# Kernel tuning notes

Measured on AMD Instinct MI355X. Metric: run time of the kernel, lower is better.

Reference implementation:

```python
import jax, jax.numpy as jnp
import numpy as np

B, S, D, H = 2, 4096, 512, 4
HD = D // H          # head_dim = key_size = value_size = 128
BLK = 512            # mask_block_size (tri-block-diagonal mask)


def setup_inputs() -> dict:
    key = jax.random.key(0)
    ks = jax.random.split(key, 7)
    # tri-block-diagonal boolean mask: query block attends to itself and adjacent blocks
    blk = np.arange(S) // BLK
    mask = np.abs(blk[:, None] - blk[None, :]) <= 1
    w_scale = 1.0 / np.sqrt(D)  # ~ variance_scaling fan_in init magnitude
    return {
        "q_input": jax.random.normal(ks[0], (B, S, D), jnp.float32),
        "kv_input": jax.random.normal(ks[1], (B, S, D), jnp.float32),
        "Wq": jax.random.normal(ks[2], (D, H * HD), jnp.float32) * w_scale,
        "Wk": jax.random.normal(ks[3], (D, H * HD), jnp.float32) * w_scale,
        "Wv": jax.random.normal(ks[4], (D, H * HD), jnp.float32) * w_scale,
        "Wo": jax.random.normal(ks[5], (H * HD, D), jnp.float32) * w_scale,
        "bo": jnp.zeros((D,), jnp.float32),
        "mask": jnp.asarray(mask),
    }


def reference(q_input, kv_input, Wq, Wk, Wv, Wo, bo, mask):
    b, s, _ = q_input.shape
    # multihead projections -> [b, s, H, HD]
    q = (q_input @ Wq).reshape(b, s, H, HD)
    k = (kv_input @ Wk).reshape(b, s, H, HD)
    v = (kv_input @ Wv).reshape(b, s, H, HD)
    # normalize_q=True: scale by key_size**-0.5 (no tanh soft cap)
    q = q * (HD ** -0.5)
    # masked attention (splash attention math): [b, H, sq, sk]
    scores = jnp.einsum("bqhd,bkhd->bhqk", q, k)
    neg = jnp.finfo(scores.dtype).min
    scores = jnp.where(mask[None, None], scores, neg)
    p = jax.nn.softmax(scores, axis=-1)
    out = jnp.einsum("bhqk,bkhd->bqhd", p, v)
    out = out.reshape(b, s, H * HD)
    return out @ Wo + bo
```

## Files before the change

kernel.cpp:

```cpp
#include <hip/hip_runtime.h>
#include <hip/hip_bf16.h>

#define S_LEN 4096
#define D_MODEL 512
#define NHEADS 4
#define HEAD_DIM 128
#define BATCH 2
#define M_ROWS 8192

typedef unsigned short u16;
typedef __attribute__((ext_vector_type(8))) short bf16x8;
typedef __attribute__((ext_vector_type(4))) short bf16x4;
typedef __attribute__((ext_vector_type(4))) float f32x4;

__device__ __forceinline__ float bf2f(u16 u) {
    return __uint_as_float(((unsigned)u) << 16);
}
__device__ __forceinline__ short f2b(float f) {
    unsigned x = __float_as_uint(f);
    unsigned r = (x + 0x7fffu + ((x >> 16) & 1u)) >> 16;
    return (short)r;
}

__device__ __forceinline__ int detect_f32(const u16* u, int nelem, int tid, int* s_cnt) {
    if (tid == 0) *s_cnt = 0;
    __syncthreads();
    int samp = nelem < 4096 ? nelem : 4096;
    int c = 0;
    for (int i = tid; i < samp; i += 256) {
        float af = fabsf(bf2f(u[i]));
        if (af != 0.0f && (!(af <= 1e12f) || af < 1e-12f)) c++;
    }
    atomicAdd(s_cnt, c);
    __syncthreads();
    return *s_cnt > 16;
}

__global__ __launch_bounds__(256) void prep_w(const void* w0, const void* w1,
                                              const void* w2, const void* w3, u16* wt) {
    __shared__ int s_cnt;
    __shared__ float tile[32][33];
    const int tid = threadIdx.x;
    const int wi = blockIdx.x >> 8, t = blockIdx.x & 255;
    const void* W = (wi == 0) ? w0 : (wi == 1) ? w1 : (wi == 2) ? w2 : w3;
    const int f32 = detect_f32((const u16*)W, 262144, tid, &s_cnt);
    const float scale = (wi == 0) ? 0.0883883476483184f : 1.0f;
    u16* Wt = wt + (size_t)wi * D_MODEL * D_MODEL;
    const int k0 = (t >> 4) * 32, n0 = (t & 15) * 32;
    const int tx = tid & 31, ty = tid >> 5;
#pragma unroll
    for (int i = 0; i < 4; i++) {
        int r = ty + 8 * i;
        long long off = (long long)(k0 + r) * D_MODEL + n0 + tx;
        float v = f32 ? ((const float*)W)[off] : bf2f(((const u16*)W)[off]);
        tile[r][tx] = v * scale;
    }
    __syncthreads();
#pragma unroll
    for (int i = 0; i < 4; i++) {
        int r = ty + 8 * i;
        Wt[(size_t)(n0 + r) * D_MODEL + k0 + tx] = (u16)f2b(tile[tx][r]);
    }
}

__global__ __launch_bounds__(256) void proj_mfma(const void* qin, const void* kvin,
                                                 const u16* wt, u16* qb, u16* kb,
                                                 u16* vbT) {
    __shared__ int s_cnt;
    __shared__ short As[128][72];
    __shared__ short Ws[128][72];
    const int z = blockIdx.z;
    const void* A = (z == 0) ? qin : kvin;
    const u16* Wt = wt + (size_t)z * 262144;
    const int tid = threadIdx.x;
    const int f32a = detect_f32((const u16*)A, 4194304, tid, &s_cnt);
    const int row0 = blockIdx.x * 128, col0 = blockIdx.y * 128;
    const int srow = tid >> 1, sk0 = (tid & 1) * 32;
    const int lane = tid & 63, wid = tid >> 6;
    const int wm = wid >> 1, wn = wid & 1;
    const int l16 = lane & 15, quad = lane >> 4;

    f32x4 acc[4][4];
#pragma unroll
    for (int i = 0; i < 4; i++)
#pragma unroll
        for (int j = 0; j < 4; j++) acc[i][j] = (f32x4){0.f, 0.f, 0.f, 0.f};

    for (int k0 = 0; k0 < D_MODEL; k0 += 64) {
        if (f32a) {
            const float* ap = (const float*)A + (size_t)(row0 + srow) * D_MODEL + k0 + sk0;
            short s[32];
#pragma unroll
            for (int i = 0; i < 8; i++) {
                f32x4 t = *(const f32x4*)(ap + 4 * i);
                s[4 * i] = f2b(t.x); s[4 * i + 1] = f2b(t.y);
                s[4 * i + 2] = f2b(t.z); s[4 * i + 3] = f2b(t.w);
            }
#pragma unroll
            for (int i = 0; i < 4; i++)
                *(bf16x8*)&As[srow][sk0 + 8 * i] = *(bf16x8*)(s + 8 * i);
        } else {
            const u16* ap = (const u16*)A + (size_t)(row0 + srow) * D_MODEL + k0 + sk0;
#pragma unroll
            for (int i = 0; i < 4; i++)
                *(bf16x8*)&As[srow][sk0 + 8 * i] = *(const bf16x8*)(ap + 8 * i);
        }
        {
            const u16* wp = Wt + (size_t)(col0 + srow) * D_MODEL + k0 + sk0;
#pragma unroll
            for (int i = 0; i < 4; i++)
                *(bf16x8*)&Ws[srow][sk0 + 8 * i] = *(const bf16x8*)(wp + 8 * i);
        }
        __syncthreads();
#pragma unroll
        for (int kc = 0; kc < 2; kc++) {
            bf16x8 af[4], bfr[4];
#pragma unroll
            for (int i = 0; i < 4; i++)
                af[i] = *(const bf16x8*)&As[wm * 64 + i * 16 + l16][kc * 32 + quad * 8];
#pragma unroll
            for (int j = 0; j < 4; j++)
                bfr[j] = *(const bf16x8*)&Ws[wn * 64 + j * 16 + l16][kc * 32 + quad * 8];
#pragma unroll
            for (int i = 0; i < 4; i++)
#pragma unroll
                for (int j = 0; j < 4; j++)
                    acc[i][j] = __builtin_amdgcn_mfma_f32_16x16x32_bf16(af[i], bfr[j],
                                                                       acc[i][j], 0, 0, 0);
        }
        __syncthreads();
    }
    if (z == 2) {
#pragma unroll
        for (int i = 0; i < 4; i++) {
            int grow = row0 + wm * 64 + i * 16 + quad * 4;
            int b = grow >> 12, s = grow & (S_LEN - 1);
#pragma unroll
            for (int j = 0; j < 4; j++) {
                int gcol = col0 + wn * 64 + j * 16 + l16;
                int h = gcol >> 7, d = gcol & 127;
                short v[4];
#pragma unroll
                for (int r = 0; r < 4; r++) v[r] = f2b(acc[i][j][r]);
                *(bf16x4*)&vbT[((size_t)(b * NHEADS + h) * HEAD_DIM + d) * S_LEN + s] =
                    *(bf16x4*)v;
            }
        }
    } else {
        u16* out = (z == 0) ? qb : kb;
#pragma unroll
        for (int i = 0; i < 4; i++) {
            int grow = row0 + wm * 64 + i * 16 + quad * 4;
#pragma unroll
            for (int j = 0; j < 4; j++) {
                int gcol = col0 + wn * 64 + j * 16 + l16;
                int h = gcol >> 7, d = gcol & 127;
#pragma unroll
                for (int r = 0; r < 4; r++) {
                    int row = grow + r;
                    int b = row >> 12, s = row & (S_LEN - 1);
                    out[((size_t)(b * NHEADS + h) * S_LEN + s) * HEAD_DIM + d] =
                        (u16)f2b(acc[i][j][r]);
                }
            }
        }
    }
}

__global__ __launch_bounds__(256, 3) void attn_mfma(const u16* qb, const u16* kb,
                                                    const u16* vbT, u16* op0, u16* op1,
                                                    u16* op2, float* lp) {
    __shared__ short Ks[32][136];
    __shared__ short Vs[128][40];
    const int bid = blockIdx.x;
    const int bh = bid & 7;
    const int rest = bid >> 3;
    const int qt = rest / 3;
    const int p3 = rest - qt * 3;
    const int q0 = qt << 7;
    const int qblk = q0 >> 9;
    const int kstart0 = (qblk == 0) ? 0 : ((qblk - 1) << 9);
    const int kend0 = (qblk == 7) ? S_LEN : ((qblk + 2) << 9);
    const int kcount = kend0 - kstart0;
    const int third = (kcount / 3) & ~31;
    const int rem32 = (kcount - 3 * third) >> 5;
    const int kstart = kstart0 + p3 * third + (p3 < rem32 ? p3 : rem32) * 32;
    const int klen = third + (p3 < rem32 ? 32 : 0);
    const int tid = threadIdx.x;
    const int lane = tid & 63, wid = tid >> 6;
    const int l16 = lane & 15, quad = lane >> 4;
    const u16* qp = qb + (size_t)bh * S_LEN * HEAD_DIM;
    const u16* kp = kb + (size_t)bh * S_LEN * HEAD_DIM;
    const u16* vp = vbT + (size_t)bh * HEAD_DIM * S_LEN;

    bf16x8 qf[2][4];
    {
        const int r = tid >> 3, c0 = (tid & 7) * 16;
        for (int c = 0; c < 4; c++) {
            const u16* src = qp + (size_t)(q0 + c * 32 + r) * HEAD_DIM + c0;
            *(bf16x8*)&Ks[r][c0] = *(const bf16x8*)src;
            *(bf16x8*)&Ks[r][c0 + 8] = *(const bf16x8*)(src + 8);
            __syncthreads();
            if (wid == c) {
#pragma unroll
                for (int i = 0; i < 2; i++)
#pragma unroll
                    for (int kc = 0; kc < 4; kc++)
                        qf[i][kc] = *(const bf16x8*)&Ks[i * 16 + l16][kc * 32 + quad * 8];
            }
            __syncthreads();
        }
    }

    f32x4 o[2][8], lacc[2];
#pragma unroll
    for (int i = 0; i < 2; i++) {
        lacc[i] = (f32x4){0.f, 0.f, 0.f, 0.f};
#pragma unroll
        for (int n = 0; n < 8; n++) o[i][n] = (f32x4){0.f, 0.f, 0.f, 0.f};
    }
    bf16x8 ones;
#pragma unroll
    for (int t = 0; t < 8; t++) ones[t] = (short)0x3F80;

    const int krow = tid >> 3, kc0 = (tid & 7) * 16;
    const int kperm = ((krow >> 2) & 1) * 16 + (krow >> 3) * 4 + (krow & 3);
    const int vd = tid >> 1, vc0 = (tid & 1) * 16;

    for (int kk = 0; kk < klen; kk += 32) {
        const int kt = kstart + kk;
        __syncthreads();
        {
            const u16* src = kp + (size_t)(kt + krow) * HEAD_DIM + kc0;
            *(bf16x8*)&Ks[kperm][kc0] = *(const bf16x8*)src;
            *(bf16x8*)&Ks[kperm][kc0 + 8] = *(const bf16x8*)(src + 8);
        }
        {
            const u16* src = vp + (size_t)vd * S_LEN + kt + vc0;
            *(bf16x8*)&Vs[vd][vc0] = *(const bf16x8*)src;
            *(bf16x8*)&Vs[vd][vc0 + 8] = *(const bf16x8*)(src + 8);
        }
        __syncthreads();
        f32x4 sa[2][2];
#pragma unroll
        for (int ki = 0; ki < 2; ki++)
#pragma unroll
            for (int qi = 0; qi < 2; qi++) sa[ki][qi] = (f32x4){0.f, 0.f, 0.f, 0.f};
#pragma unroll
        for (int kc = 0; kc < 4; kc++) {
            bf16x8 kf0 = *(const bf16x8*)&Ks[l16][kc * 32 + quad * 8];
            bf16x8 kf1 = *(const bf16x8*)&Ks[16 + l16][kc * 32 + quad * 8];
#pragma unroll
            for (int qi = 0; qi < 2; qi++) {
                sa[0][qi] = __builtin_amdgcn_mfma_f32_16x16x32_bf16(kf0, qf[qi][kc], sa[0][qi], 0, 0, 0);
                sa[1][qi] = __builtin_amdgcn_mfma_f32_16x16x32_bf16(kf1, qf[qi][kc], sa[1][qi], 0, 0, 0);
            }
        }
        bf16x8 pfrag[2];
#pragma unroll
        for (int qi = 0; qi < 2; qi++) {
            short pv[8];
#pragma unroll
            for (int ki = 0; ki < 2; ki++)
#pragma unroll
                for (int r = 0; r < 4; r++)
                    pv[ki * 4 + r] = f2b(__expf(sa[ki][qi][r] - 8.0f));
            pfrag[qi] = *(bf16x8*)pv;
            lacc[qi] = __builtin_amdgcn_mfma_f32_16x16x32_bf16(ones, pfrag[qi], lacc[qi], 0, 0, 0);
        }
#pragma unroll
        for (int n = 0; n < 8; n++) {
            bf16x8 vf = *(const bf16x8*)&Vs[n * 16 + l16][quad * 8];
#pragma unroll
            for (int qi = 0; qi < 2; qi++)
                o[qi][n] = __builtin_amdgcn_mfma_f32_16x16x32_bf16(vf, pfrag[qi], o[qi][n], 0, 0, 0);
        }
    }
    u16* op = (p3 == 0) ? op0 : (p3 == 1 ? op1 : op2);
#pragma unroll
    for (int qi = 0; qi < 2; qi++) {
        size_t gq = (size_t)bh * S_LEN + q0 + wid * 32 + qi * 16 + l16;
#pragma unroll
        for (int n = 0; n < 8; n++) {
            short v[4];
#pragma unroll
            for (int r = 0; r < 4; r++) v[r] = f2b(o[qi][n][r]);
            *(bf16x4*)&op[gq * HEAD_DIM + n * 16 + quad * 4] = *(bf16x4*)v;
        }
        if (quad == 0) lp[(size_t)p3 * 8 * S_LEN + gq] = lacc[qi][0];
    }
}

__global__ __launch_bounds__(256) void outproj_mfma(const u16* op0, const u16* op1,
                                                    const u16* op2, const float* lp,
                                                    const u16* Wt, const void* bias,
                                                    float* out) {
    __shared__ int s_cnt;
    __shared__ short As[64][72];
    __shared__ short Ws[128][72];
    const int tid = threadIdx.x;
    const int f32b = detect_f32((const u16*)bias, 512, tid, &s_cnt);
    const int row0 = blockIdx.x * 64, col0 = blockIdx.y * 128;
    const int lane = tid & 63, wid = tid >> 6;
    const int wm = wid >> 1, wn = wid & 1;
    const int l16 = lane & 15, quad = lane >> 4;
    const int sr = tid >> 2, sk = (tid & 3) * 16;
    const int wr = tid >> 1, wk = (tid & 1) * 32;
    const size_t N = (size_t)8 * S_LEN;
    const int arow = row0 + sr;
    const int ab = arow >> 12, as = arow & (S_LEN - 1);
    f32x4 acc[2][4];
#pragma unroll
    for (int i = 0; i < 2; i++)
#pragma unroll
        for (int j = 0; j < 4; j++) acc[i][j] = (f32x4){0.f, 0.f, 0.f, 0.f};

    for (int k0 = 0; k0 < D_MODEL; k0 += 64) {
        {
            const int h = (k0 + sk) >> 7, d = (k0 + sk) & 127;
            const size_t gq = (size_t)(ab * NHEADS + h) * S_LEN + as;
            float inv = 1.0f / (lp[gq] + lp[N + gq] + lp[2 * N + gq]);
            const size_t base = gq * HEAD_DIM + d;
            bf16x8 a0 = *(const bf16x8*)&op0[base];
            bf16x8 a1 = *(const bf16x8*)&op1[base];
            bf16x8 a2 = *(const bf16x8*)&op2[base];
            bf16x8 b0 = *(const bf16x8*)&op0[base + 8];
            bf16x8 b1 = *(const bf16x8*)&op1[base + 8];
            bf16x8 b2 = *(const bf16x8*)&op2[base + 8];
            short v[16];
#pragma unroll
            for (int i = 0; i < 8; i++) {
                v[i] = f2b((bf2f((u16)a0[i]) + bf2f((u16)a1[i]) + bf2f((u16)a2[i])) * inv);
                v[8 + i] = f2b((bf2f((u16)b0[i]) + bf2f((u16)b1[i]) + bf2f((u16)b2[i])) * inv);
            }
            *(bf16x8*)&As[sr][sk] = *(bf16x8*)v;
            *(bf16x8*)&As[sr][sk + 8] = *(bf16x8*)(v + 8);
        }
        {
            const u16* wp = Wt + (size_t)(col0 + wr) * D_MODEL + k0 + wk;
#pragma unroll
            for (int i = 0; i < 4; i++)
                *(bf16x8*)&Ws[wr][wk + 8 * i] = *(const bf16x8*)(wp + 8 * i);
        }
        __syncthreads();
#pragma unroll
        for (int kc = 0; kc < 2; kc++) {
            bf16x8 af[2], bfr[4];
#pragma unroll
            for (int i = 0; i < 2; i++)
                af[i] = *(const bf16x8*)&As[wm * 32 + i * 16 + l16][kc * 32 + quad * 8];
#pragma unroll
            for (int j = 0; j < 4; j++)
                bfr[j] = *(const bf16x8*)&Ws[wn * 64 + j * 16 + l16][kc * 32 + quad * 8];
#pragma unroll
            for (int i = 0; i < 2; i++)
#pragma unroll
                for (int j = 0; j < 4; j++)
                    acc[i][j] = __builtin_amdgcn_mfma_f32_16x16x32_bf16(af[i], bfr[j],
                                                                       acc[i][j], 0, 0, 0);
        }
        __syncthreads();
    }
#pragma unroll
    for (int i = 0; i < 2; i++) {
        int grow = row0 + wm * 32 + i * 16 + quad * 4;
#pragma unroll
        for (int j = 0; j < 4; j++) {
            int gcol = col0 + wn * 64 + j * 16 + l16;
            float bval = f32b ? ((const float*)bias)[gcol] : bf2f(((const u16*)bias)[gcol]);
#pragma unroll
            for (int r = 0; r < 4; r++)
                out[(size_t)(grow + r) * D_MODEL + gcol] = acc[i][j][r] + bval;
        }
    }
}

extern "C" void kernel_launch(void* const* d_in, const int* in_sizes, int n_in,
                              void* d_out, int out_size, void* d_ws, size_t ws_size,
                              hipStream_t stream) {
    (void)in_sizes; (void)out_size; (void)ws_size; (void)n_in;
    const void* q_input = d_in[0];
    const void* kv_input = d_in[1];
    const void* Wq = d_in[2];
    const void* Wk = d_in[3];
    const void* Wv = d_in[4];
    const void* Wo = d_in[5];
    const void* bo = d_in[6];

    const size_t NELEM = (size_t)M_ROWS * D_MODEL;
    u16* wt = (u16*)d_ws;
    u16* qb = wt + 4 * 262144;
    u16* kb = qb + NELEM;
    u16* vbT = kb + NELEM;
    u16* op0 = vbT + NELEM;
    u16* op1 = op0 + NELEM;
    u16* op2 = op1 + NELEM;
    float* lp = (float*)(op2 + NELEM);

    prep_w<<<1024, 256, 0, stream>>>(Wq, Wk, Wv, Wo, wt);
    proj_mfma<<<dim3(64, 4, 3), 256, 0, stream>>>(q_input, kv_input, wt, qb, kb, vbT);
    attn_mfma<<<8 * 32 * 3, 256, 0, stream>>>(qb, kb, vbT, op0, op1, op2, lp);
    outproj_mfma<<<dim3(128, 4), 256, 0, stream>>>(op0, op1, op2, lp, wt + 3 * 262144,
                                                   bo, (float*)d_out);
}
```

Measured before the change: 246.8 us.

## Halve projection row tile and double attention key tile to 64

The projection GEMM now uses 64-row tiles instead of 128, doubling the grid to 1536 blocks so more CUs are occupied. The attention kernel processes 64 keys per iteration instead of 32, using larger K/V shared tiles and two score groups per step. This halves the number of barriers and tile loads in the attention loop. In exchange it raises LDS and register use, which could reduce occupancy under launch_bounds(256,3), and the smaller projection tile reuses each weight tile across fewer rows.

New measurement: 229.8 us. 1.07x faster.

```diff
diff --git a/kernel.cpp b/kernel.cpp
--- a/kernel.cpp
+++ b/kernel.cpp
@@ -67,62 +67,61 @@
                                                  const u16* wt, u16* qb, u16* kb,
                                                  u16* vbT) {
     __shared__ int s_cnt;
-    __shared__ short As[128][72];
+    __shared__ short As[64][72];
     __shared__ short Ws[128][72];
     const int z = blockIdx.z;
     const void* A = (z == 0) ? qin : kvin;
     const u16* Wt = wt + (size_t)z * 262144;
     const int tid = threadIdx.x;
     const int f32a = detect_f32((const u16*)A, 4194304, tid, &s_cnt);
-    const int row0 = blockIdx.x * 128, col0 = blockIdx.y * 128;
-    const int srow = tid >> 1, sk0 = (tid & 1) * 32;
+    const int row0 = blockIdx.x * 64, col0 = blockIdx.y * 128;
     const int lane = tid & 63, wid = tid >> 6;
     const int wm = wid >> 1, wn = wid & 1;
     const int l16 = lane & 15, quad = lane >> 4;
-
-    f32x4 acc[4][4];
-#pragma unroll
-    for (int i = 0; i < 4; i++)
+    const int ar = tid >> 2, ak = (tid & 3) * 16;
+    const int wr = tid >> 1, wk = (tid & 1) * 32;
+
+    f32x4 acc[2][4];
+#pragma unroll
+    for (int i = 0; i < 2; i++)
 #pragma unroll
         for (int j = 0; j < 4; j++) acc[i][j] = (f32x4){0.f, 0.f, 0.f, 0.f};
 
     for (int k0 = 0; k0 < D_MODEL; k0 += 64) {
         if (f32a) {
-            const float* ap = (const float*)A + (size_t)(row0 + srow) * D_MODEL + k0 + sk0;
-            short s[32];
-#pragma unroll
-            for (int i = 0; i < 8; i++) {
+            const float* ap = (const float*)A + (size_t)(row0 + ar) * D_MODEL + k0 + ak;
+            short s[16];
+#pragma unroll
+            for (int i = 0; i < 4; i++) {
                 f32x4 t = *(const f32x4*)(ap + 4 * i);
                 s[4 * i] = f2b(t.x); s[4 * i + 1] = f2b(t.y);
                 s[4 * i + 2] = f2b(t.z); s[4 * i + 3] = f2b(t.w);
             }
+            *(bf16x8*)&As[ar][ak] = *(bf16x8*)s;
+            *(bf16x8*)&As[ar][ak + 8] = *(bf16x8*)(s + 8);
+        } else {
+            const u16* ap = (const u16*)A + (size_t)(row0 + ar) * D_MODEL + k0 + ak;
+            *(bf16x8*)&As[ar][ak] = *(const bf16x8*)ap;
+            *(bf16x8*)&As[ar][ak + 8] = *(const bf16x8*)(ap + 8);
+        }
+        {
+            const u16* wp = Wt + (size_t)(col0 + wr) * D_MODEL + k0 + wk;
 #pragma unroll
             for (int i = 0; i < 4; i++)
-                *(bf16x8*)&As[srow][sk0 + 8 * i] = *(bf16x8*)(s + 8 * i);
-        } else {
-            const u16* ap = (const u16*)A + (size_t)(row0 + srow) * D_MODEL + k0 + sk0;
-#pragma unroll
-            for (int i = 0; i < 4; i++)
-                *(bf16x8*)&As[srow][sk0 + 8 * i] = *(const bf16x8*)(ap + 8 * i);
-        }
-        {
-            const u16* wp = Wt + (size_t)(col0 + srow) * D_MODEL + k0 + sk0;
-#pragma unroll
-            for (int i = 0; i < 4; i++)
-                *(bf16x8*)&Ws[srow][sk0 + 8 * i] = *(const bf16x8*)(wp + 8 * i);
+                *(bf16x8*)&Ws[wr][wk + 8 * i] = *(const bf16x8*)(wp + 8 * i);
         }
         __syncthreads();
 #pragma unroll
         for (int kc = 0; kc < 2; kc++) {
-            bf16x8 af[4], bfr[4];
-#pragma unroll
-            for (int i = 0; i < 4; i++)
-                af[i] = *(const bf16x8*)&As[wm * 64 + i * 16 + l16][kc * 32 + quad * 8];
+            bf16x8 af[2], bfr[4];
+#pragma unroll
+            for (int i = 0; i < 2; i++)
+                af[i] = *(const bf16x8*)&As[wm * 32 + i * 16 + l16][kc * 32 + quad * 8];
 #pragma unroll
             for (int j = 0; j < 4; j++)
                 bfr[j] = *(const bf16x8*)&Ws[wn * 64 + j * 16 + l16][kc * 32 + quad * 8];
 #pragma unroll
-            for (int i = 0; i < 4; i++)
+            for (int i = 0; i < 2; i++)
 #pragma unroll
                 for (int j = 0; j < 4; j++)
                     acc[i][j] = __builtin_amdgcn_mfma_f32_16x16x32_bf16(af[i], bfr[j],
@@ -132,8 +131,8 @@
     }
     if (z == 2) {
 #pragma unroll
-        for (int i = 0; i < 4; i++) {
-            int grow = row0 + wm * 64 + i * 16 + quad * 4;
+        for (int i = 0; i < 2; i++) {
+            int grow = row0 + wm * 32 + i * 16 + quad * 4;
             int b = grow >> 12, s = grow & (S_LEN - 1);
 #pragma unroll
             for (int j = 0; j < 4; j++) {
@@ -149,8 +148,8 @@
     } else {
         u16* out = (z == 0) ? qb : kb;
 #pragma unroll
-        for (int i = 0; i < 4; i++) {
-            int grow = row0 + wm * 64 + i * 16 + quad * 4;
+        for (int i = 0; i < 2; i++) {
+            int grow = row0 + wm * 32 + i * 16 + quad * 4;
 #pragma unroll
             for (int j = 0; j < 4; j++) {
                 int gcol = col0 + wn * 64 + j * 16 + l16;
@@ -170,8 +169,8 @@
 __global__ __launch_bounds__(256, 3) void attn_mfma(const u16* qb, const u16* kb,
                                                     const u16* vbT, u16* op0, u16* op1,
                                                     u16* op2, float* lp) {
-    __shared__ short Ks[32][136];
-    __shared__ short Vs[128][40];
+    __shared__ short Ks[64][136];
+    __shared__ short Vs[128][72];
     const int bid = blockIdx.x;
     const int bh = bid & 7;
     const int rest = bid >> 3;
@@ -182,10 +181,10 @@
     const int kstart0 = (qblk == 0) ? 0 : ((qblk - 1) << 9);
     const int kend0 = (qblk == 7) ? S_LEN : ((qblk + 2) << 9);
     const int kcount = kend0 - kstart0;
-    const int third = (kcount / 3) & ~31;
-    const int rem32 = (kcount - 3 * third) >> 5;
-    const int kstart = kstart0 + p3 * third + (p3 < rem32 ? p3 : rem32) * 32;
-    const int klen = third + (p3 < rem32 ? 32 : 0);
+    const int third = (kcount / 3) & ~63;
+    const int rem64 = (kcount - 3 * third) >> 6;
+    const int kstart = kstart0 + p3 * third + (p3 < rem64 ? p3 : rem64) * 64;
+    const int klen = third + (p3 < rem64 ? 64 : 0);
     const int tid = threadIdx.x;
     const int lane = tid & 63, wid = tid >> 6;
     const int l16 = lane & 15, quad = lane >> 4;
@@ -195,18 +194,20 @@
 
     bf16x8 qf[2][4];
     {
-        const int r = tid >> 3, c0 = (tid & 7) * 16;
-        for (int c = 0; c < 4; c++) {
-            const u16* src = qp + (size_t)(q0 + c * 32 + r) * HEAD_DIM + c0;
-            *(bf16x8*)&Ks[r][c0] = *(const bf16x8*)src;
-            *(bf16x8*)&Ks[r][c0 + 8] = *(const bf16x8*)(src + 8);
+        const int r = tid >> 2, c0 = (tid & 3) * 32;
+        for (int c = 0; c < 2; c++) {
+            const u16* src = qp + (size_t)(q0 + c * 64 + r) * HEAD_DIM + c0;
+#pragma unroll
+            for (int i = 0; i < 4; i++)
+                *(bf16x8*)&Ks[r][c0 + 8 * i] = *(const bf16x8*)(src + 8 * i);
             __syncthreads();
-            if (wid == c) {
-#pragma unroll
-                for (int i = 0; i < 2; i++)
+            if ((wid >> 1) == c) {
+#pragma unroll
+                for (int qi = 0; qi < 2; qi++)
 #pragma unroll
                     for (int kc = 0; kc < 4; kc++)
-                        qf[i][kc] = *(const bf16x8*)&Ks[i * 16 + l16][kc * 32 + quad * 8];
+                        qf[qi][kc] = *(const bf16x8*)
+                            &Ks[(wid & 1) * 32 + qi * 16 + l16][kc * 32 + quad * 8];
             }
             __syncthreads();
         }
@@ -223,57 +224,68 @@
 #pragma unroll
     for (int t = 0; t < 8; t++) ones[t] = (short)0x3F80;
 
-    const int krow = tid >> 3, kc0 = (tid & 7) * 16;
-    const int kperm = ((krow >> 2) & 1) * 16 + (krow >> 3) * 4 + (krow & 3);
-    const int vd = tid >> 1, vc0 = (tid & 1) * 16;
-
-    for (int kk = 0; kk < klen; kk += 32) {
+    const int krow = tid >> 2, kc0 = (tid & 3) * 32;
+    const int kperm = (krow & 32) | (((krow >> 2) & 1) << 4) | (((krow >> 3) & 3) << 2) |
+                      (krow & 3);
+    const int vd = tid >> 1, vc0 = (tid & 1) * 32;
+
+    for (int kk = 0; kk < klen; kk += 64) {
         const int kt = kstart + kk;
         __syncthreads();
         {
             const u16* src = kp + (size_t)(kt + krow) * HEAD_DIM + kc0;
-            *(bf16x8*)&Ks[kperm][kc0] = *(const bf16x8*)src;
-            *(bf16x8*)&Ks[kperm][kc0 + 8] = *(const bf16x8*)(src + 8);
+#pragma unroll
+            for (int i = 0; i < 4; i++)
+                *(bf16x8*)&Ks[kperm][kc0 + 8 * i] = *(const bf16x8*)(src + 8 * i);
         }
         {
             const u16* src = vp + (size_t)vd * S_LEN + kt + vc0;
-            *(bf16x8*)&Vs[vd][vc0] = *(const bf16x8*)src;
-            *(bf16x8*)&Vs[vd][vc0 + 8] = *(const bf16x8*)(src + 8);
-        }
-        __syncthreads();
-        f32x4 sa[2][2];
-#pragma unroll
-        for (int ki = 0; ki < 2; ki++)
-#pragma unroll
-            for (int qi = 0; qi < 2; qi++) sa[ki][qi] = (f32x4){0.f, 0.f, 0.f, 0.f};
-#pragma unroll
-        for (int kc = 0; kc < 4; kc++) {
-            bf16x8 kf0 = *(const bf16x8*)&Ks[l16][kc * 32 + quad * 8];
-            bf16x8 kf1 = *(const bf16x8*)&Ks[16 + l16][kc * 32 + quad * 8];
+#pragma unroll
+            for (int i = 0; i < 4; i++)
+                *(bf16x8*)&Vs[vd][vc0 + 8 * i] = *(const bf16x8*)(src + 8 * i);
+        }
+        __syncthreads();
+        bf16x8 pfrag[2][2];
+#pragma unroll
+        for (int g = 0; g < 2; g++) {
+            f32x4 sa[2][2];
+#pragma unroll
+            for (int ki = 0; ki < 2; ki++)
+#pragma unroll
+                for (int qi = 0; qi < 2; qi++) sa[ki][qi] = (f32x4){0.f, 0.f, 0.f, 0.f};
+#pragma unroll
+            for (int kc = 0; kc < 4; kc++) {
+                bf16x8 kf0 = *(const bf16x8*)&Ks[g * 32 + l16][kc * 32 + quad * 8];
+                bf16x8 kf1 = *(const bf16x8*)&Ks[g * 32 + 16 + l16][kc * 32 + quad * 8];
+#pragma unroll
+                for (int qi = 0; qi < 2; qi++) {
+                    sa[0][qi] = __builtin_amdgcn_mfma_f32_16x16x32_bf16(kf0, qf[qi][kc], sa[0][qi], 0, 0, 0);
+                    sa[1][qi] = __builtin_amdgcn_mfma_f32_16x16x32_bf16(kf1, qf[qi][kc], sa[1][qi], 0, 0, 0);
+                }
+            }
 #pragma unroll
             for (int qi = 0; qi < 2; qi++) {
-                sa[0][qi] = __builtin_amdgcn_mfma_f32_16x16x32_bf16(kf0, qf[qi][kc], sa[0][qi], 0, 0, 0);
-                sa[1][qi] = __builtin_amdgcn_mfma_f32_16x16x32_bf16(kf1, qf[qi][kc], sa[1][qi], 0, 0, 0);
-            }
-        }
-        bf16x8 pfrag[2];
-#pragma unroll
-        for (int qi = 0; qi < 2; qi++) {
-            short pv[8];
-#pragma unroll
-            for (int ki = 0; ki < 2; ki++)
-#pragma unroll
-                for (int r = 0; r < 4; r++)
-                    pv[ki * 4 + r] = f2b(__expf(sa[ki][qi][r] - 8.0f));
-            pfrag[qi] = *(bf16x8*)pv;
-            lacc[qi] = __builtin_amdgcn_mfma_f32_16x16x32_bf16(ones, pfrag[qi], lacc[qi], 0, 0, 0);
+                short pv[8];
+#pragma unroll
+                for (int ki = 0; ki < 2; ki++)
+#pragma unroll
+                    for (int r = 0; r < 4; r++)
+                        pv[ki * 4 + r] = f2b(__expf(sa[ki][qi][r] - 8.0f));
+                pfrag[g][qi] = *(bf16x8*)pv;
+                lacc[qi] = __builtin_amdgcn_mfma_f32_16x16x32_bf16(ones, pfrag[g][qi],
+                                                                  lacc[qi], 0, 0, 0);
+            }
         }
 #pragma unroll
         for (int n = 0; n < 8; n++) {
-            bf16x8 vf = *(const bf16x8*)&Vs[n * 16 + l16][quad * 8];
-#pragma unroll
-            for (int qi = 0; qi < 2; qi++)
-                o[qi][n] = __builtin_amdgcn_mfma_f32_16x16x32_bf16(vf, pfrag[qi], o[qi][n], 0, 0, 0);
+#pragma unroll
+            for (int g = 0; g < 2; g++) {
+                bf16x8 vf = *(const bf16x8*)&Vs[n * 16 + l16][g * 32 + quad * 8];
+#pragma unroll
+                for (int qi = 0; qi < 2; qi++)
+                    o[qi][n] = __builtin_amdgcn_mfma_f32_16x16x32_bf16(vf, pfrag[g][qi],
+                                                                      o[qi][n], 0, 0, 0);
+            }
         }
     }
     u16* op = (p3 == 0) ? op0 : (p3 == 1 ? op1 : op2);
@@ -398,7 +410,7 @@
     float* lp = (float*)(op2 + NELEM);
 
     prep_w<<<1024, 256, 0, stream>>>(Wq, Wk, Wv, Wo, wt);
-    proj_mfma<<<dim3(64, 4, 3), 256, 0, stream>>>(q_input, kv_input, wt, qb, kb, vbT);
+    proj_mfma<<<dim3(128, 4, 3), 256, 0, stream>>>(q_input, kv_input, wt, qb, kb, vbT);
     attn_mfma<<<8 * 32 * 3, 256, 0, stream>>>(qb, kb, vbT, op0, op1, op2, lp);
     outproj_mfma<<<dim3(128, 4), 256, 0, stream>>>(op0, op1, op2, lp, wt + 3 * 262144,
                                                    bo, (float*)d_out);
```
